# Kernel tuning notes

Hardware: AMD Instinct MI355X
Metric: run time of the kernel (lower is better)

Reference implementation:

```python
import jax, jax.numpy as jnp
import numpy as np

N = 100000      # nodes
E = 1600000     # edges
F_IN = 128
HID = 64
N_CLS = 40


def setup_inputs() -> dict:
    key = jax.random.key(0)
    ks = jax.random.split(key, 8)
    x = jax.random.normal(ks[0], (N, F_IN), dtype=jnp.float32)
    edge_index = jax.random.randint(ks[1], (2, E), 0, N, dtype=jnp.int64)
    # SAGEConv params: lin_l (applied to mean-aggregated neighbors, with bias),
    # lin_r (applied to root/self features, no bias). Glorot-ish init scaling.
    W1_l = jax.random.normal(ks[2], (F_IN, HID), dtype=jnp.float32) / np.sqrt(F_IN)
    b1 = jnp.zeros((HID,), dtype=jnp.float32)
    W1_r = jax.random.normal(ks[3], (F_IN, HID), dtype=jnp.float32) / np.sqrt(F_IN)
    W2_l = jax.random.normal(ks[4], (HID, N_CLS), dtype=jnp.float32) / np.sqrt(HID)
    b2 = jnp.zeros((N_CLS,), dtype=jnp.float32)
    W2_r = jax.random.normal(ks[5], (HID, N_CLS), dtype=jnp.float32) / np.sqrt(HID)
    return {"x": x, "edge_index": edge_index,
            "W1_l": W1_l, "b1": b1, "W1_r": W1_r,
            "W2_l": W2_l, "b2": b2, "W2_r": W2_r}


def _sage_conv(x, src, dst, W_l, b_l, W_r):
    # mean aggregation of neighbor features: messages flow src -> dst
    msgs = x[src]                                              # [E, d]
    summed = jax.ops.segment_sum(msgs, dst, num_segments=N)    # [N, d]
    cnt = jax.ops.segment_sum(jnp.ones((src.shape[0],), x.dtype), dst,
                              num_segments=N)                  # [N]
    agg = summed / jnp.maximum(cnt, 1.0)[:, None]
    return agg @ W_l + b_l + x @ W_r


def reference(x, edge_index, W1_l, b1, W1_r, W2_l, b2, W2_r):
    src, dst = edge_index[0], edge_index[1]
    h = jax.nn.relu(_sage_conv(x, src, dst, W1_l, b1, W1_r))
    # dropout: identity in eval mode
    logits = _sage_conv(h, src, dst, W2_l, b2, W2_r)
    return jax.nn.log_softmax(logits, axis=1)
```

## Files before the change

kernel.cpp:

```cpp
#include <hip/hip_runtime.h>
#include <math.h>

#define N_NODES 100000
#define F_IN    128
#define HID     64
#define N_CLS   40
#define MT      (N_NODES / 16)

#define BSHIFT  9
#define BSZ     512
#define NB      ((N_NODES + BSZ - 1) / BSZ)
#define EPB     4096

typedef __attribute__((ext_vector_type(8))) short bf8_t;
typedef __attribute__((ext_vector_type(4))) float f4_t;
typedef __attribute__((ext_vector_type(2))) float f2v_t;

typedef unsigned short ushort_t;
typedef unsigned int uint_t;
typedef unsigned char uchar_t;

__device__ __forceinline__ ushort_t f2b(float f) {
    union { float f; uint_t u; } c; c.f = f;
    uint_t u = c.u + 0x7FFFu + ((c.u >> 16) & 1u);
    return (ushort_t)(u >> 16);
}
__device__ __forceinline__ float b2f(ushort_t h) {
    union { uint_t u; float f; } c; c.u = ((uint_t)h) << 16;
    return c.f;
}

#if defined(__has_builtin)
#if __has_builtin(__builtin_amdgcn_cvt_pk_f32_fp8) && __has_builtin(__builtin_amdgcn_cvt_pk_fp8_f32)
#define HAVE_FP8_HW 1
#endif
#endif

__device__ __forceinline__ uchar_t fp8_enc(float v) {
#ifdef HAVE_FP8_HW
    return (uchar_t)(__builtin_amdgcn_cvt_pk_fp8_f32(v, v, 0, false) & 0xff);
#else
    union { float f; uint_t u; } c; c.f = v;
    uint_t s = c.u >> 31;
    float av = fabsf(v);
    if (av > 448.f) av = 448.f;
    int e;
    float m = frexpf(av, &e);
    int ee = e + 6;
    uchar_t r;
    if (av == 0.f) r = 0;
    else if (ee <= 0) {
        int q = (int)(av * 512.f + 0.5f);
        if (q > 7) q = 7;
        r = (uchar_t)q;
    } else {
        int q = (int)(m * 16.f + 0.5f);
        if (q == 16) { q = 8; ee += 1; }
        if (ee > 15) { ee = 15; q = 15; }
        r = (uchar_t)((ee << 3) | (q & 7));
    }
    return r | (uchar_t)(s << 7);
#endif
}

__device__ __forceinline__ f2v_t fp8x2_dec_lo(uint_t w) {
#ifdef HAVE_FP8_HW
    return __builtin_amdgcn_cvt_pk_f32_fp8(w, false);
#else
    f2v_t r;
    for (int k = 0; k < 2; ++k) {
        uchar_t b = (w >> (8 * k)) & 0xff;
        uint_t s = (b >> 7) & 1, e = (b >> 3) & 15, m = b & 7;
        float f;
        if (e) { union { uint_t u; float ff; } c;
                 c.u = (s << 31) | ((e + 120) << 23) | (m << 20); f = c.ff; }
        else   { f = (float)m * 0.001953125f; if (s) f = -f; }
        r[k] = f;
    }
    return r;
#endif
}
__device__ __forceinline__ f2v_t fp8x2_dec_hi(uint_t w) {
#ifdef HAVE_FP8_HW
    return __builtin_amdgcn_cvt_pk_f32_fp8(w, true);
#else
    return fp8x2_dec_lo(w >> 16);
#endif
}

__global__ void block_hist_kernel(const int* __restrict__ ei, int E,
                                  int* __restrict__ blockHist) {
    __shared__ int cnt[NB];
    int t = threadIdx.x, blk = blockIdx.x;
    for (int i = t; i < NB; i += 256) cnt[i] = 0;
    __syncthreads();
    int e0 = blk * EPB;
#pragma unroll
    for (int i = 0; i < EPB / 256; ++i) {
        int e = e0 + i * 256 + t;
        if (e < E) atomicAdd(&cnt[ei[E + e] >> BSHIFT], 1);
    }
    __syncthreads();
    for (int i = t; i < NB; i += 256) blockHist[blk * NB + i] = cnt[i];
}

__global__ void col_scan_kernel(const int* __restrict__ blockHist, int nblk,
                                int* __restrict__ blockBase,
                                int* __restrict__ btot) {
    __shared__ int ss[256];
    __shared__ int carry;
    int bin = blockIdx.x, t = threadIdx.x;
    if (t == 0) carry = 0;
    __syncthreads();
    for (int c0 = 0; c0 < nblk; c0 += 256) {
        int b = c0 + t;
        int v = (b < nblk) ? blockHist[b * NB + bin] : 0;
        ss[t] = v;
        __syncthreads();
        for (int off = 1; off < 256; off <<= 1) {
            int u = (t >= off) ? ss[t - off] : 0;
            __syncthreads();
            ss[t] += u;
            __syncthreads();
        }
        if (b < nblk) blockBase[b * NB + bin] = carry + ss[t] - v;
        __syncthreads();
        if (t == 255) carry += ss[255];
        __syncthreads();
    }
    if (t == 0) btot[bin] = carry;
}

__global__ void bucket_scan_kernel(const int* __restrict__ btot,
                                   int* __restrict__ boff,
                                   int* __restrict__ rowptr) {
    __shared__ int ss[256];
    int t = threadIdx.x;
    int v = (t < NB) ? btot[t] : 0;
    ss[t] = v;
    __syncthreads();
    for (int off = 1; off < 256; off <<= 1) {
        int u = (t >= off) ? ss[t - off] : 0;
        __syncthreads();
        ss[t] += u;
        __syncthreads();
    }
    if (t < NB) boff[t] = ss[t] - v;
    if (t == NB - 1) rowptr[N_NODES] = ss[t];
}

__global__ void scatter_pairs_kernel(const int* __restrict__ ei, int E,
                                     const int* __restrict__ blockBase,
                                     const int* __restrict__ boff,
                                     uint_t* __restrict__ pairs) {
    __shared__ int cur[NB];
    __shared__ int base[NB];
    int t = threadIdx.x, blk = blockIdx.x;
    for (int i = t; i < NB; i += 256) {
        cur[i] = 0;
        base[i] = boff[i] + blockBase[blk * NB + i];
    }
    __syncthreads();
    int e0 = blk * EPB;
#pragma unroll
    for (int i = 0; i < EPB / 256; ++i) {
        int e = e0 + i * 256 + t;
        if (e < E) {
            int src = ei[e];
            int dst = ei[E + e];
            int bin = dst >> BSHIFT;
            int r = atomicAdd(&cur[bin], 1);
            pairs[base[bin] + r] = ((uint_t)src << BSHIFT) | (uint_t)(dst & (BSZ - 1));
        }
    }
}

__global__ void bucket_sort_kernel(const uint_t* __restrict__ pairs,
                                   const int* __restrict__ boff,
                                   const int* __restrict__ btot,
                                   int* __restrict__ rowptr,
                                   int* __restrict__ csr) {
    __shared__ int hist[BSZ];
    __shared__ int lofs[BSZ];
    int bin = blockIdx.x, t = threadIdx.x;
    int base = boff[bin], cnt = btot[bin];
    hist[t] = 0;
    __syncthreads();
    for (int i = t; i < cnt; i += BSZ)
        atomicAdd(&hist[pairs[base + i] & (BSZ - 1)], 1);
    __syncthreads();
    int v = hist[t];
    lofs[t] = v;
    __syncthreads();
    for (int off = 1; off < BSZ; off <<= 1) {
        int u = (t >= off) ? lofs[t - off] : 0;
        __syncthreads();
        lofs[t] += u;
        __syncthreads();
    }
    int excl = lofs[t] - v;
    int d_global = (bin << BSHIFT) + t;
    if (d_global < N_NODES) rowptr[d_global] = base + excl;
    __syncthreads();
    lofs[t] = excl;
    hist[t] = 0;
    __syncthreads();
    for (int i = t; i < cnt; i += BSZ) {
        uint_t p = pairs[base + i];
        int lb = p & (BSZ - 1);
        int r = atomicAdd(&hist[lb], 1);
        csr[base + lofs[lb] + r] = (int)(p >> BSHIFT);
    }
}

__global__ void cvt_w_kernel(const float* __restrict__ W1l,
                             const float* __restrict__ W1r,
                             const float* __restrict__ W2l,
                             const float* __restrict__ W2r,
                             ushort_t* __restrict__ W1t,
                             ushort_t* __restrict__ W2t) {
    int t = blockIdx.x * blockDim.x + threadIdx.x;
    if (t < 128 * F_IN) {
        int n = t / F_IN, k = t - n * F_IN;
        float v = (n < HID) ? W1l[k * HID + n] : W1r[k * HID + (n - HID)];
        W1t[t] = f2b(v);
    } else if (t < 128 * F_IN + 80 * HID) {
        int u = t - 128 * F_IN;
        int n = u / HID, k = u - n * HID;
        float v = (n < N_CLS) ? W2l[k * N_CLS + n] : W2r[k * N_CLS + (n - N_CLS)];
        W2t[u] = f2b(v);
    }
}

__global__ void gemm1_mfma_kernel(const float* __restrict__ x,
                                  const ushort_t* __restrict__ W1t,
                                  uchar_t* __restrict__ y1f8,
                                  ushort_t* __restrict__ z1b) {
    int gid = blockIdx.x * blockDim.x + threadIdx.x;
    int wave = gid >> 6, lane = gid & 63;
    if (wave >= MT) return;
    int m0 = wave * 16;
    int r = lane & 15, q = lane >> 4;

    const float* xr = x + (size_t)(m0 + r) * F_IN + q * 8;
    bf8_t a[4];
#pragma unroll
    for (int kt = 0; kt < 4; ++kt) {
        float4 u = *(const float4*)(xr + kt * 32);
        float4 v = *(const float4*)(xr + kt * 32 + 4);
        bf8_t t;
        t[0] = (short)f2b(u.x); t[1] = (short)f2b(u.y);
        t[2] = (short)f2b(u.z); t[3] = (short)f2b(u.w);
        t[4] = (short)f2b(v.x); t[5] = (short)f2b(v.y);
        t[6] = (short)f2b(v.z); t[7] = (short)f2b(v.w);
        a[kt] = t;
    }
#pragma unroll
    for (int tn = 0; tn < 8; ++tn) {
        const ushort_t* wr = W1t + (size_t)(tn * 16 + r) * F_IN + q * 8;
        f4_t acc = {0.f, 0.f, 0.f, 0.f};
#pragma unroll
        for (int kt = 0; kt < 4; ++kt) {
            bf8_t b = *(const bf8_t*)(wr + kt * 32);
            acc = __builtin_amdgcn_mfma_f32_16x16x32_bf16(a[kt], b, acc, 0, 0, 0);
        }
        int col = tn * 16 + r;
        if (col < HID) {
#pragma unroll
            for (int rr = 0; rr < 4; ++rr) {
                int row = m0 + q * 4 + rr;
                y1f8[(size_t)row * HID + col] = fp8_enc(acc[rr]);
            }
        } else {
#pragma unroll
            for (int rr = 0; rr < 4; ++rr) {
                int row = m0 + q * 4 + rr;
                z1b[(size_t)row * HID + (col - HID)] = f2b(acc[rr]);
            }
        }
    }
}

__global__ void agg1_kernel(const int* __restrict__ rowptr,
                            const int* __restrict__ csr,
                            const uchar_t* __restrict__ y1f8,
                            const ushort_t* __restrict__ z1b,
                            const float* __restrict__ b1,
                            ushort_t* __restrict__ hb) {
    int gid = blockIdx.x * blockDim.x + threadIdx.x;
    int wave = gid >> 6, lane = gid & 63;
    int g = lane >> 4, l = lane & 15;
    int n = wave * 4 + g;
    if (n >= N_NODES) return;
    int beg = rowptr[n], end = rowptr[n + 1];
    float a0 = 0.f, a1 = 0.f, a2 = 0.f, a3 = 0.f;
    int i = beg;
    for (; i + 1 < end; i += 2) {
        int s0 = csr[i], s1 = csr[i + 1];
        uint_t w0 = *(const uint_t*)(y1f8 + (size_t)s0 * HID + l * 4);
        uint_t w1 = *(const uint_t*)(y1f8 + (size_t)s1 * HID + l * 4);
        f2v_t p0 = fp8x2_dec_lo(w0), p1 = fp8x2_dec_hi(w0);
        f2v_t q0 = fp8x2_dec_lo(w1), q1 = fp8x2_dec_hi(w1);
        a0 += p0[0] + q0[0];
        a1 += p0[1] + q0[1];
        a2 += p1[0] + q1[0];
        a3 += p1[1] + q1[1];
    }
    if (i < end) {
        uint_t w = *(const uint_t*)(y1f8 + (size_t)csr[i] * HID + l * 4);
        f2v_t p0 = fp8x2_dec_lo(w), p1 = fp8x2_dec_hi(w);
        a0 += p0[0]; a1 += p0[1]; a2 += p1[0]; a3 += p1[1];
    }
    float inv = 1.0f / fmaxf((float)(end - beg), 1.0f);
    float4 bb = *(const float4*)(b1 + l * 4);
    ushort4 zz = *(const ushort4*)(z1b + (size_t)n * HID + l * 4);
    float r0 = fmaxf(fmaf(a0, inv, bb.x + b2f(zz.x)), 0.f);
    float r1 = fmaxf(fmaf(a1, inv, bb.y + b2f(zz.y)), 0.f);
    float r2 = fmaxf(fmaf(a2, inv, bb.z + b2f(zz.z)), 0.f);
    float r3 = fmaxf(fmaf(a3, inv, bb.w + b2f(zz.w)), 0.f);
    ushort4 o;
    o.x = f2b(r0); o.y = f2b(r1); o.z = f2b(r2); o.w = f2b(r3);
    *(ushort4*)(hb + (size_t)n * HID + l * 4) = o;
}

__global__ void gemm2_mfma_kernel(const ushort_t* __restrict__ hb,
                                  const ushort_t* __restrict__ W2t,
                                  uchar_t* __restrict__ y2f8,
                                  ushort_t* __restrict__ z2b) {
    int gid = blockIdx.x * blockDim.x + threadIdx.x;
    int wave = gid >> 6, lane = gid & 63;
    if (wave >= MT) return;
    int m0 = wave * 16;
    int r = lane & 15, q = lane >> 4;

    const ushort_t* hr = hb + (size_t)(m0 + r) * HID + q * 8;
    bf8_t a[2];
#pragma unroll
    for (int kt = 0; kt < 2; ++kt)
        a[kt] = *(const bf8_t*)(hr + kt * 32);

#pragma unroll
    for (int tn = 0; tn < 5; ++tn) {
        const ushort_t* wr = W2t + (size_t)(tn * 16 + r) * HID + q * 8;
        f4_t acc = {0.f, 0.f, 0.f, 0.f};
#pragma unroll
        for (int kt = 0; kt < 2; ++kt) {
            bf8_t b = *(const bf8_t*)(wr + kt * 32);
            acc = __builtin_amdgcn_mfma_f32_16x16x32_bf16(a[kt], b, acc, 0, 0, 0);
        }
        int col = tn * 16 + r;
        if (col < N_CLS) {
#pragma unroll
            for (int rr = 0; rr < 4; ++rr) {
                int row = m0 + q * 4 + rr;
                y2f8[(size_t)row * HID + col] = fp8_enc(acc[rr]);
            }
        } else {
#pragma unroll
            for (int rr = 0; rr < 4; ++rr) {
                int row = m0 + q * 4 + rr;
                z2b[(size_t)row * HID + (col - N_CLS)] = f2b(acc[rr]);
            }
        }
    }
}

__global__ void agg2_kernel(const int* __restrict__ rowptr,
                            const int* __restrict__ csr,
                            const uchar_t* __restrict__ y2f8,
                            const ushort_t* __restrict__ z2b,
                            const float* __restrict__ b2,
                            float* __restrict__ out) {
    int gid = blockIdx.x * blockDim.x + threadIdx.x;
    int wave = gid >> 6, lane = gid & 63;
    int g = lane >> 4, l = lane & 15;
    int n = wave * 4 + g;
    if (n >= N_NODES) return;
    int beg = rowptr[n], end = rowptr[n + 1];
    float a0 = 0.f, a1 = 0.f, a2 = 0.f, a3 = 0.f;
    int i = beg;
    for (; i + 1 < end; i += 2) {
        int s0 = csr[i], s1 = csr[i + 1];
        uint_t w0 = *(const uint_t*)(y2f8 + (size_t)s0 * HID + l * 4);
        uint_t w1 = *(const uint_t*)(y2f8 + (size_t)s1 * HID + l * 4);
        f2v_t p0 = fp8x2_dec_lo(w0), p1 = fp8x2_dec_hi(w0);
        f2v_t q0 = fp8x2_dec_lo(w1), q1 = fp8x2_dec_hi(w1);
        a0 += p0[0] + q0[0];
        a1 += p0[1] + q0[1];
        a2 += p1[0] + q1[0];
        a3 += p1[1] + q1[1];
    }
    if (i < end) {
        uint_t w = *(const uint_t*)(y2f8 + (size_t)csr[i] * HID + l * 4);
        f2v_t p0 = fp8x2_dec_lo(w), p1 = fp8x2_dec_hi(w);
        a0 += p0[0]; a1 += p0[1]; a2 += p1[0]; a3 += p1[1];
    }
    float inv = 1.0f / fmaxf((float)(end - beg), 1.0f);
    int c0 = l * 4;
    float4 bb = (l < 10) ? *(const float4*)(b2 + c0)
                         : make_float4(0.f, 0.f, 0.f, 0.f);
    ushort4 zz = *(const ushort4*)(z2b + (size_t)n * HID + c0);
    float v0 = (c0 + 0 < N_CLS) ? fmaf(a0, inv, bb.x + b2f(zz.x)) : -INFINITY;
    float v1 = (c0 + 1 < N_CLS) ? fmaf(a1, inv, bb.y + b2f(zz.y)) : -INFINITY;
    float v2 = (c0 + 2 < N_CLS) ? fmaf(a2, inv, bb.z + b2f(zz.z)) : -INFINITY;
    float v3 = (c0 + 3 < N_CLS) ? fmaf(a3, inv, bb.w + b2f(zz.w)) : -INFINITY;

    float m = fmaxf(fmaxf(v0, v1), fmaxf(v2, v3));
#pragma unroll
    for (int off = 1; off < 16; off <<= 1)
        m = fmaxf(m, __shfl_xor(m, off, 64));
    float s = 0.f;
    if (v0 > -INFINITY) s += expf(v0 - m);
    if (v1 > -INFINITY) s += expf(v1 - m);
    if (v2 > -INFINITY) s += expf(v2 - m);
    if (v3 > -INFINITY) s += expf(v3 - m);
#pragma unroll
    for (int off = 1; off < 16; off <<= 1)
        s += __shfl_xor(s, off, 64);
    float ls = logf(s);
    if (l < 10) {
        float4 o = make_float4(v0 - m - ls, v1 - m - ls, v2 - m - ls, v3 - m - ls);
        *(float4*)(out + (size_t)n * N_CLS + c0) = o;
    }
}

extern "C" void kernel_launch(void* const* d_in, const int* in_sizes, int n_in,
                              void* d_out, int out_size, void* d_ws, size_t ws_size,
                              hipStream_t stream) {
    const float* x   = (const float*)d_in[0];
    const int*   ei  = (const int*)d_in[1];
    const float* W1l = (const float*)d_in[2];
    const float* b1  = (const float*)d_in[3];
    const float* W1r = (const float*)d_in[4];
    const float* W2l = (const float*)d_in[5];
    const float* b2  = (const float*)d_in[6];
    const float* W2r = (const float*)d_in[7];
    float* out = (float*)d_out;
    const int E = in_sizes[1] / 2;
    const int nblk = (E + EPB - 1) / EPB;

    char* p = (char*)d_ws;
    auto take = [&](size_t bytes) {
        char* q = p;
        p += (bytes + 15) & ~(size_t)15;
        return (void*)q;
    };
    int* rowptr     = (int*)take(sizeof(int) * (N_NODES + 4));
    int* blockHist  = (int*)take(sizeof(int) * (size_t)nblk * NB);
    int* blockBase  = (int*)take(sizeof(int) * (size_t)nblk * NB);
    int* btot       = (int*)take(sizeof(int) * NB);
    int* boff       = (int*)take(sizeof(int) * NB);
    uint_t* pairs   = (uint_t*)take(sizeof(uint_t) * (size_t)E);
    int* csr        = (int*)take(sizeof(int) * (size_t)E);
    ushort_t* W1t   = (ushort_t*)take(sizeof(ushort_t) * 128 * F_IN);
    ushort_t* W2t   = (ushort_t*)take(sizeof(ushort_t) * 80 * HID);
    uchar_t* y1f8   = (uchar_t*)take(sizeof(uchar_t) * (size_t)N_NODES * HID);
    ushort_t* z1b   = (ushort_t*)take(sizeof(ushort_t) * (size_t)N_NODES * HID);
    ushort_t* hb    = (ushort_t*)take(sizeof(ushort_t) * (size_t)N_NODES * HID);
    uchar_t* y2f8 = y1f8;
    ushort_t* z2b = z1b;

    const int B = 256;

    block_hist_kernel<<<nblk, 256, 0, stream>>>(ei, E, blockHist);
    col_scan_kernel<<<NB, 256, 0, stream>>>(blockHist, nblk, blockBase, btot);
    bucket_scan_kernel<<<1, 256, 0, stream>>>(btot, boff, rowptr);
    scatter_pairs_kernel<<<nblk, 256, 0, stream>>>(ei, E, blockBase, boff, pairs);
    bucket_sort_kernel<<<NB, BSZ, 0, stream>>>(pairs, boff, btot, rowptr, csr);

    cvt_w_kernel<<<(128 * F_IN + 80 * HID + B - 1) / B, B, 0, stream>>>(
        W1l, W1r, W2l, W2r, W1t, W2t);

    int t_mfma = MT * 64;
    int t_agg = (N_NODES / 4) * 64;

    gemm1_mfma_kernel<<<(t_mfma + B - 1) / B, B, 0, stream>>>(x, W1t, y1f8, z1b);
    agg1_kernel<<<(t_agg + B - 1) / B, B, 0, stream>>>(rowptr, csr, y1f8, z1b, b1, hb);
    gemm2_mfma_kernel<<<(t_mfma + B - 1) / B, B, 0, stream>>>(hb, W2t, y2f8, z2b);
    agg2_kernel<<<(t_agg + B - 1) / B, B, 0, stream>>>(rowptr, csr, y2f8, z2b, b2, out);
}
```

Baseline: 270.5 us.

## Split layer-1 gather table into column halves and compact layer-2 fp8 rows

```diff
diff --git a/kernel.cpp b/kernel.cpp
--- a/kernel.cpp
+++ b/kernel.cpp
@@ -234,7 +234,8 @@
 
 __global__ void gemm1_mfma_kernel(const float* __restrict__ x,
                                   const ushort_t* __restrict__ W1t,
-                                  uchar_t* __restrict__ y1f8,
+                                  uchar_t* __restrict__ y1a,
+                                  uchar_t* __restrict__ y1b,
                                   ushort_t* __restrict__ z1b) {
     int gid = blockIdx.x * blockDim.x + threadIdx.x;
     int wave = gid >> 6, lane = gid & 63;
@@ -265,11 +266,17 @@
             acc = __builtin_amdgcn_mfma_f32_16x16x32_bf16(a[kt], b, acc, 0, 0, 0);
         }
         int col = tn * 16 + r;
-        if (col < HID) {
+        if (col < 32) {
 #pragma unroll
             for (int rr = 0; rr < 4; ++rr) {
                 int row = m0 + q * 4 + rr;
-                y1f8[(size_t)row * HID + col] = fp8_enc(acc[rr]);
+                y1a[(size_t)row * 32 + col] = fp8_enc(acc[rr]);
+            }
+        } else if (col < HID) {
+#pragma unroll
+            for (int rr = 0; rr < 4; ++rr) {
+                int row = m0 + q * 4 + rr;
+                y1b[(size_t)row * 32 + (col - 32)] = fp8_enc(acc[rr]);
             }
         } else {
 #pragma unroll
@@ -281,46 +288,51 @@
     }
 }
 
-__global__ void agg1_kernel(const int* __restrict__ rowptr,
-                            const int* __restrict__ csr,
-                            const uchar_t* __restrict__ y1f8,
-                            const ushort_t* __restrict__ z1b,
-                            const float* __restrict__ b1,
-                            ushort_t* __restrict__ hb) {
+__global__ void agg1_half_kernel(const int* __restrict__ rowptr,
+                                 const int* __restrict__ csr,
+                                 const uchar_t* __restrict__ y1h,
+                                 const ushort_t* __restrict__ z1b,
+                                 const float* __restrict__ b1,
+                                 ushort_t* __restrict__ hb, int half) {
     int gid = blockIdx.x * blockDim.x + threadIdx.x;
     int wave = gid >> 6, lane = gid & 63;
-    int g = lane >> 4, l = lane & 15;
-    int n = wave * 4 + g;
+    int g = lane >> 3, l = lane & 7;
+    int n = wave * 8 + g;
     if (n >= N_NODES) return;
     int beg = rowptr[n], end = rowptr[n + 1];
     float a0 = 0.f, a1 = 0.f, a2 = 0.f, a3 = 0.f;
     int i = beg;
-    for (; i + 1 < end; i += 2) {
-        int s0 = csr[i], s1 = csr[i + 1];
-        uint_t w0 = *(const uint_t*)(y1f8 + (size_t)s0 * HID + l * 4);
-        uint_t w1 = *(const uint_t*)(y1f8 + (size_t)s1 * HID + l * 4);
+    for (; i + 3 < end; i += 4) {
+        int s0 = csr[i], s1 = csr[i + 1], s2 = csr[i + 2], s3 = csr[i + 3];
+        uint_t w0 = *(const uint_t*)(y1h + (size_t)s0 * 32 + l * 4);
+        uint_t w1 = *(const uint_t*)(y1h + (size_t)s1 * 32 + l * 4);
+        uint_t w2 = *(const uint_t*)(y1h + (size_t)s2 * 32 + l * 4);
+        uint_t w3 = *(const uint_t*)(y1h + (size_t)s3 * 32 + l * 4);
         f2v_t p0 = fp8x2_dec_lo(w0), p1 = fp8x2_dec_hi(w0);
         f2v_t q0 = fp8x2_dec_lo(w1), q1 = fp8x2_dec_hi(w1);
-        a0 += p0[0] + q0[0];
-        a1 += p0[1] + q0[1];
-        a2 += p1[0] + q1[0];
-        a3 += p1[1] + q1[1];
-    }
-    if (i < end) {
-        uint_t w = *(const uint_t*)(y1f8 + (size_t)csr[i] * HID + l * 4);
+        f2v_t r0 = fp8x2_dec_lo(w2), r1 = fp8x2_dec_hi(w2);
+        f2v_t t0 = fp8x2_dec_lo(w3), t1 = fp8x2_dec_hi(w3);
+        a0 += (p0[0] + q0[0]) + (r0[0] + t0[0]);
+        a1 += (p0[1] + q0[1]) + (r0[1] + t0[1]);
+        a2 += (p1[0] + q1[0]) + (r1[0] + t1[0]);
+        a3 += (p1[1] + q1[1]) + (r1[1] + t1[1]);
+    }
+    for (; i < end; ++i) {
+        uint_t w = *(const uint_t*)(y1h + (size_t)csr[i] * 32 + l * 4);
         f2v_t p0 = fp8x2_dec_lo(w), p1 = fp8x2_dec_hi(w);
         a0 += p0[0]; a1 += p0[1]; a2 += p1[0]; a3 += p1[1];
     }
     float inv = 1.0f / fmaxf((float)(end - beg), 1.0f);
-    float4 bb = *(const float4*)(b1 + l * 4);
-    ushort4 zz = *(const ushort4*)(z1b + (size_t)n * HID + l * 4);
+    int c = half * 32 + l * 4;
+    float4 bb = *(const float4*)(b1 + c);
+    ushort4 zz = *(const ushort4*)(z1b + (size_t)n * HID + c);
     float r0 = fmaxf(fmaf(a0, inv, bb.x + b2f(zz.x)), 0.f);
     float r1 = fmaxf(fmaf(a1, inv, bb.y + b2f(zz.y)), 0.f);
     float r2 = fmaxf(fmaf(a2, inv, bb.z + b2f(zz.z)), 0.f);
     float r3 = fmaxf(fmaf(a3, inv, bb.w + b2f(zz.w)), 0.f);
     ushort4 o;
     o.x = f2b(r0); o.y = f2b(r1); o.z = f2b(r2); o.w = f2b(r3);
-    *(ushort4*)(hb + (size_t)n * HID + l * 4) = o;
+    *(ushort4*)(hb + (size_t)n * HID + c) = o;
 }
 
 __global__ void gemm2_mfma_kernel(const ushort_t* __restrict__ hb,
@@ -353,7 +365,7 @@
 #pragma unroll
             for (int rr = 0; rr < 4; ++rr) {
                 int row = m0 + q * 4 + rr;
-                y2f8[(size_t)row * HID + col] = fp8_enc(acc[rr]);
+                y2f8[(size_t)row * 40 + col] = fp8_enc(acc[rr]);
             }
         } else {
 #pragma unroll
@@ -379,19 +391,23 @@
     int beg = rowptr[n], end = rowptr[n + 1];
     float a0 = 0.f, a1 = 0.f, a2 = 0.f, a3 = 0.f;
     int i = beg;
-    for (; i + 1 < end; i += 2) {
-        int s0 = csr[i], s1 = csr[i + 1];
-        uint_t w0 = *(const uint_t*)(y2f8 + (size_t)s0 * HID + l * 4);
-        uint_t w1 = *(const uint_t*)(y2f8 + (size_t)s1 * HID + l * 4);
+    for (; i + 3 < end; i += 4) {
+        int s0 = csr[i], s1 = csr[i + 1], s2 = csr[i + 2], s3 = csr[i + 3];
+        uint_t w0 = *(const uint_t*)(y2f8 + (size_t)s0 * 40 + l * 4);
+        uint_t w1 = *(const uint_t*)(y2f8 + (size_t)s1 * 40 + l * 4);
+        uint_t w2 = *(const uint_t*)(y2f8 + (size_t)s2 * 40 + l * 4);
+        uint_t w3 = *(const uint_t*)(y2f8 + (size_t)s3 * 40 + l * 4);
         f2v_t p0 = fp8x2_dec_lo(w0), p1 = fp8x2_dec_hi(w0);
         f2v_t q0 = fp8x2_dec_lo(w1), q1 = fp8x2_dec_hi(w1);
-        a0 += p0[0] + q0[0];
-        a1 += p0[1] + q0[1];
-        a2 += p1[0] + q1[0];
-        a3 += p1[1] + q1[1];
-    }
-    if (i < end) {
-        uint_t w = *(const uint_t*)(y2f8 + (size_t)csr[i] * HID + l * 4);
+        f2v_t r0 = fp8x2_dec_lo(w2), r1 = fp8x2_dec_hi(w2);
+        f2v_t t0 = fp8x2_dec_lo(w3), t1 = fp8x2_dec_hi(w3);
+        a0 += (p0[0] + q0[0]) + (r0[0] + t0[0]);
+        a1 += (p0[1] + q0[1]) + (r0[1] + t0[1]);
+        a2 += (p1[0] + q1[0]) + (r1[0] + t1[0]);
+        a3 += (p1[1] + q1[1]) + (r1[1] + t1[1]);
+    }
+    for (; i < end; ++i) {
+        uint_t w = *(const uint_t*)(y2f8 + (size_t)csr[i] * 40 + l * 4);
         f2v_t p0 = fp8x2_dec_lo(w), p1 = fp8x2_dec_hi(w);
         a0 += p0[0]; a1 += p0[1]; a2 += p1[0]; a3 += p1[1];
     }
@@ -454,10 +470,11 @@
     int* csr        = (int*)take(sizeof(int) * (size_t)E);
     ushort_t* W1t   = (ushort_t*)take(sizeof(ushort_t) * 128 * F_IN);
     ushort_t* W2t   = (ushort_t*)take(sizeof(ushort_t) * 80 * HID);
-    uchar_t* y1f8   = (uchar_t*)take(sizeof(uchar_t) * (size_t)N_NODES * HID);
+    uchar_t* y1a    = (uchar_t*)take(sizeof(uchar_t) * (size_t)N_NODES * 32);
+    uchar_t* y1b    = (uchar_t*)take(sizeof(uchar_t) * (size_t)N_NODES * 32);
     ushort_t* z1b   = (ushort_t*)take(sizeof(ushort_t) * (size_t)N_NODES * HID);
     ushort_t* hb    = (ushort_t*)take(sizeof(ushort_t) * (size_t)N_NODES * HID);
-    uchar_t* y2f8 = y1f8;
+    uchar_t* y2f8 = y1a;
     ushort_t* z2b = z1b;
 
     const int B = 256;
@@ -472,10 +489,12 @@
         W1l, W1r, W2l, W2r, W1t, W2t);
 
     int t_mfma = MT * 64;
-    int t_agg = (N_NODES / 4) * 64;
-
-    gemm1_mfma_kernel<<<(t_mfma + B - 1) / B, B, 0, stream>>>(x, W1t, y1f8, z1b);
-    agg1_kernel<<<(t_agg + B - 1) / B, B, 0, stream>>>(rowptr, csr, y1f8, z1b, b1, hb);
+    int t_agg1 = (N_NODES / 8) * 64;
+    int t_agg2 = (N_NODES / 4) * 64;
+
+    gemm1_mfma_kernel<<<(t_mfma + B - 1) / B, B, 0, stream>>>(x, W1t, y1a, y1b, z1b);
+    agg1_half_kernel<<<(t_agg1 + B - 1) / B, B, 0, stream>>>(rowptr, csr, y1a, z1b, b1, hb, 0);
+    agg1_half_kernel<<<(t_agg1 + B - 1) / B, B, 0, stream>>>(rowptr, csr, y1b, z1b, b1, hb, 1);
     gemm2_mfma_kernel<<<(t_mfma + B - 1) / B, B, 0, stream>>>(hb, W2t, y2f8, z2b);
-    agg2_kernel<<<(t_agg + B - 1) / B, B, 0, stream>>>(rowptr, csr, y2f8, z2b, b2, out);
-}
+    agg2_kernel<<<(t_agg2 + B - 1) / B, B, 0, stream>>>(rowptr, csr, y2f8, z2b, b2, out);
+}
```

Result: no change. 266.9 us (-1.3%).
